# Performance work log

Hardware: AMD Instinct MI355X
Metric: run time of the kernel (lower is better)

Reference implementation:

```python
import jax, jax.numpy as jnp
import numpy as np


def _ln(x, g, b, eps=1e-5):
    m = x.mean(-1, keepdims=True)
    v = ((x - m) ** 2).mean(-1, keepdims=True)
    return (x - m) * jax.lax.rsqrt(v + eps) * g + b


def _forward(x, norm1_g, norm1_b, in_proj_w, conv_w, x_proj_w, dt_projs_w,
             dt_projs_b, A_logs, Ds, out_norm_g, out_norm_b, out_proj_w,
             norm2_g, norm2_b, fc1_w, fc1_b, fc2_w, fc2_b):
    B, C, H, W = x.shape
    z = jnp.transpose(x, (0, 2, 3, 1))  # (B,H,W,C)

    # ---- SS2D branch (forward_type='v3noz': no z gate) ----
    u = _ln(z, norm1_g, norm1_b)
    u = u @ in_proj_w.T                       # (B,H,W,Din)
    Din = u.shape[-1]
    uc = jnp.transpose(u, (0, 3, 1, 2))       # (B,Din,H,W)
    uc = jax.lax.conv_general_dilated(
        uc, conv_w, (1, 1), 'SAME', feature_group_count=Din,
        dimension_numbers=('NCHW', 'OIHW', 'NCHW'))
    uc = jax.nn.silu(uc)

    L = H * W
    K = x_proj_w.shape[0]                     # 4 scan directions
    R = dt_projs_w.shape[-1]                  # dt_rank
    N = (x_proj_w.shape[1] - R) // 2          # d_state

    # cross-scan: row-major, col-major, and their reversals
    xf = uc.reshape(B, Din, L)
    xt = jnp.transpose(uc, (0, 1, 3, 2)).reshape(B, Din, L)
    xs = jnp.stack([xf, xt, xf[..., ::-1], xt[..., ::-1]], axis=1)  # (B,K,Din,L)

    dbl = jnp.einsum('bkdl,kcd->bkcl', xs, x_proj_w)
    dts, Bs, Cs = jnp.split(dbl, [R, R + N], axis=2)  # (B,K,R,L),(B,K,N,L),(B,K,N,L)
    dt = jax.nn.softplus(jnp.einsum('bkrl,kdr->bkdl', dts, dt_projs_w)
                         + dt_projs_b[None, :, :, None])  # (B,K,Din,L)
    A = -jnp.exp(A_logs).reshape(K, Din, N)

    # selective scan: h_t = exp(dt*A)*h_{t-1} + dt*B_t*u_t; via associative scan
    a = jnp.exp(dt[:, :, :, None, :] * A[None, :, :, :, None])          # (B,K,Din,N,L)
    bb = dt[:, :, :, None, :] * Bs[:, :, None, :, :] * xs[:, :, :, None, :]

    def comb(e1, e2):
        a1, b1 = e1
        a2, b2 = e2
        return a2 * a1, a2 * b1 + b2

    _, h = jax.lax.associative_scan(comb, (a, bb), axis=-1)
    y = jnp.einsum('bkdnl,bknl->bkdl', h, Cs) + Ds.reshape(K, Din)[None, :, :, None] * xs

    # cross-merge: undo reversals / transpose, then sum
    yr = y[:, 0] + y[:, 2][..., ::-1]
    yt = jnp.transpose((y[:, 1] + y[:, 3][..., ::-1]).reshape(B, Din, W, H),
                       (0, 1, 3, 2)).reshape(B, Din, L)
    ym = jnp.transpose((yr + yt).reshape(B, Din, H, W), (0, 2, 3, 1))  # (B,H,W,Din)

    ym = _ln(ym, out_norm_g, out_norm_b)
    z = z + ym @ out_proj_w.T

    # ---- MLP branch ----
    m = _ln(z, norm2_g, norm2_b)
    m = jax.nn.gelu(m @ fc1_w.T + fc1_b, approximate=False) @ fc2_w.T + fc2_b
    z = z + m

    # outer wrapper residual
    return x + jnp.transpose(z, (0, 3, 1, 2))


def setup_inputs() -> dict:
    key = jax.random.key(0)
    ks = jax.random.split(key, 10)
    dims, Din, R, N, K, dmlp = 96, 192, 6, 1, 4, 384
    B, H, W = 4, 64, 64
    f32 = jnp.float32
    return {
        'x': jax.random.normal(ks[0], (B, dims, H, W), f32),
        'norm1_g': jnp.ones((dims,), f32),
        'norm1_b': jnp.zeros((dims,), f32),
        'in_proj_w': jax.random.normal(ks[1], (Din, dims), f32) * 0.02,
        'conv_w': jax.random.normal(ks[2], (Din, 1, 3, 3), f32) * 0.1,
        'x_proj_w': jax.random.normal(ks[3], (K, R + 2 * N, Din), f32) * 0.02,
        'dt_projs_w': jax.random.normal(ks[4], (K, Din, R), f32) * 0.1,
        'dt_projs_b': jax.random.uniform(ks[5], (K, Din), f32) * 0.1,
        'A_logs': jnp.zeros((K * Din, N), f32),  # v0 init: A=arange(1,N+1) -> log=0 for N=1
        'Ds': jnp.ones((K * Din,), f32),
        'out_norm_g': jnp.ones((Din,), f32),
        'out_norm_b': jnp.zeros((Din,), f32),
        'out_proj_w': jax.random.normal(ks[6], (dims, Din), f32) * 0.02,
        'norm2_g': jnp.ones((dims,), f32),
        'norm2_b': jnp.zeros((dims,), f32),
        'fc1_w': jax.random.normal(ks[7], (dmlp, dims), f32) * 0.02,
        'fc1_b': jnp.zeros((dmlp,), f32),
        'fc2_w': jax.random.normal(ks[8], (dims, dmlp), f32) * 0.02,
        'fc2_b': jnp.zeros((dims,), f32),
    }


def reference(x, norm1_g, norm1_b, in_proj_w, conv_w, x_proj_w, dt_projs_w,
              dt_projs_b, A_logs, Ds, out_norm_g, out_norm_b, out_proj_w,
              norm2_g, norm2_b, fc1_w, fc1_b, fc2_w, fc2_b):
    return _forward(x, norm1_g, norm1_b, in_proj_w, conv_w, x_proj_w,
                    dt_projs_w, dt_projs_b, A_logs, Ds, out_norm_g, out_norm_b,
                    out_proj_w, norm2_g, norm2_b, fc1_w, fc1_b, fc2_w, fc2_b)
```

## Files before the change

kernel.cpp:

```cpp
#include <hip/hip_runtime.h>
#include <math.h>

namespace {

constexpr int Bn = 4, Cn = 96, Hn = 64, Wn = 64, Ln = 4096, Din = 192;
constexpr int Kn = 4, Rn = 6, Dmlp = 384;
constexpr int NCH = 128, CLEN = 32;

typedef short short8 __attribute__((ext_vector_type(8)));
typedef float f32x4 __attribute__((ext_vector_type(4)));

__device__ __forceinline__ float softplusf_(float x) {
  return fmaxf(x, 0.f) + __logf(1.f + __expf(-fabsf(x)));
}
__device__ __forceinline__ float siluf_(float x) {
  return x / (1.f + __expf(-x));
}
__device__ __forceinline__ float geluf_(float x) {
  return 0.5f * x * (1.f + erff(x * 0.7071067811865476f));
}
__device__ __forceinline__ unsigned short f2bf(float f) {
  unsigned u = __float_as_uint(f);
  unsigned r = 0x7fffu + ((u >> 16) & 1u);
  return (unsigned short)((u + r) >> 16);
}
__device__ __forceinline__ float bf2f(unsigned short v) {
  return __uint_as_float(((unsigned)v) << 16);
}

__global__ __launch_bounds__(256) void k1_ln_inproj(
    const float* __restrict__ x, const float* __restrict__ gam,
    const float* __restrict__ bet, const float* __restrict__ win,
    const float* __restrict__ w1, const float* __restrict__ w2,
    const float* __restrict__ wout, const float* __restrict__ wxp,
    unsigned short* __restrict__ ucpb, unsigned short* __restrict__ w1b,
    unsigned short* __restrict__ w2b, unsigned short* __restrict__ woutb,
    unsigned short* __restrict__ wxpb) {
  const int tid = threadIdx.x;
  if (blockIdx.x >= 512) {
    int t = (blockIdx.x - 512) * 256 + tid;
    if (t < 36864) w1b[t] = f2bf(w1[t]);
    else if (t < 73728) w2b[t - 36864] = f2bf(w2[t - 36864]);
    else if (t < 92160) woutb[t - 73728] = f2bf(wout[t - 73728]);
    else wxpb[t - 92160] = f2bf(wxp[t - 92160]);
    return;
  }

  __shared__ float sx[32 * 97];
  __shared__ __align__(16) unsigned short smb[32 * 104];
  __shared__ __align__(16) unsigned short swin[192 * 96];
  const int p0 = blockIdx.x * 32;
  const int b = p0 >> 12, pl0 = p0 & (Ln - 1);

  for (int e = tid; e < 4608; e += 256) {
    float4 w4 = reinterpret_cast<const float4*>(win)[e];
    uint2 pk;
    pk.x = (unsigned)f2bf(w4.x) | ((unsigned)f2bf(w4.y) << 16);
    pk.y = (unsigned)f2bf(w4.z) | ((unsigned)f2bf(w4.w) << 16);
    *reinterpret_cast<uint2*>(&swin[e * 4]) = pk;
  }

  for (int f = tid; f < 32 * 96; f += 256) {
    int c = f >> 5, pp = f & 31;
    sx[pp * 97 + c] = x[((size_t)b * Cn + c) * Ln + pl0 + pp];
  }
  __syncthreads();
  {
    const int pp = tid >> 3, t8 = tid & 7;
    float s = 0.f;
    for (int c = t8 * 12; c < t8 * 12 + 12; ++c) s += sx[pp * 97 + c];
    s += __shfl_xor(s, 1, 8); s += __shfl_xor(s, 2, 8); s += __shfl_xor(s, 4, 8);
    float m = s * (1.f / 96.f);
    float v = 0.f;
    for (int c = t8 * 12; c < t8 * 12 + 12; ++c) {
      float t = sx[pp * 97 + c] - m; v += t * t;
    }
    v += __shfl_xor(v, 1, 8); v += __shfl_xor(v, 2, 8); v += __shfl_xor(v, 4, 8);
    float rs = rsqrtf(v * (1.f / 96.f) + 1e-5f);
    for (int c = t8 * 12; c < t8 * 12 + 12; ++c)
      sx[pp * 97 + c] = (sx[pp * 97 + c] - m) * rs * gam[c] + bet[c];
  }
  __syncthreads();
  for (int f = tid; f < 32 * 96; f += 256) {
    int pp = f / 96, c = f % 96;
    smb[pp * 104 + c] = f2bf(sx[pp * 97 + c]);
  }
  __syncthreads();

  const int wv = tid >> 6, lane = tid & 63;
  const int l15 = lane & 15, lhi = lane >> 4;
  const int mt = wv & 1, nbase = (wv >> 1) * 6;
  for (int t = 0; t < 6; ++t) {
    const int n0 = (nbase + t) * 16;
    f32x4 acc = {0.f, 0.f, 0.f, 0.f};
#pragma unroll
    for (int kk = 0; kk < 3; ++kk) {
      short8 av = *reinterpret_cast<const short8*>(
          &smb[(16 * mt + l15) * 104 + kk * 32 + lhi * 8]);
      short8 bv = *reinterpret_cast<const short8*>(
          &swin[(n0 + l15) * 96 + kk * 32 + lhi * 8]);
      acc = __builtin_amdgcn_mfma_f32_16x16x32_bf16(av, bv, acc, 0, 0, 0);
    }
    const int j = n0 + l15;
    uint2 pk;
    pk.x = (unsigned)f2bf(acc[0]) | ((unsigned)f2bf(acc[1]) << 16);
    pk.y = (unsigned)f2bf(acc[2]) | ((unsigned)f2bf(acc[3]) << 16);
    *reinterpret_cast<uint2*>(
        &ucpb[((size_t)b * Din + j) * Ln + pl0 + 16 * mt + lhi * 4]) = pk;
  }
}

__global__ __launch_bounds__(512) void k2a_conv(
    const unsigned short* __restrict__ ucpb, const float* __restrict__ cw,
    unsigned short* __restrict__ utb) {
  __shared__ float su[64 * 97];
  const int tid = threadIdx.x;
  const int bid = blockIdx.x;
  const int half = bid & 1, bh = bid >> 1;
  const int b = bh >> 6, h = bh & 63;
  const int w = tid & 63, wg = tid >> 6;
  const int d0 = half * 96;

  for (int dd = 0; dd < 12; ++dd) {
    int dl = wg * 12 + dd;
    int d = d0 + dl;
    const unsigned short* base = &ucpb[((size_t)b * Din + d) * Ln];
    float r0 = (h > 0) ? bf2f(base[(h - 1) * 64 + w]) : 0.f;
    float r1 = bf2f(base[h * 64 + w]);
    float r2 = (h < 63) ? bf2f(base[(h + 1) * 64 + w]) : 0.f;
    const float* wt = &cw[d * 9];
    float rl, rr, acc;
    rl = __shfl(r0, (w + 63) & 63); if (w == 0) rl = 0.f;
    rr = __shfl(r0, (w + 1) & 63);  if (w == 63) rr = 0.f;
    acc = rl * wt[0] + r0 * wt[1] + rr * wt[2];
    rl = __shfl(r1, (w + 63) & 63); if (w == 0) rl = 0.f;
    rr = __shfl(r1, (w + 1) & 63);  if (w == 63) rr = 0.f;
    acc += rl * wt[3] + r1 * wt[4] + rr * wt[5];
    rl = __shfl(r2, (w + 63) & 63); if (w == 0) rl = 0.f;
    rr = __shfl(r2, (w + 1) & 63);  if (w == 63) rr = 0.f;
    acc += rl * wt[6] + r2 * wt[7] + rr * wt[8];
    su[w * 97 + dl] = siluf_(acc);
  }
  __syncthreads();

  for (int f = tid; f < 768; f += 512) {
    int pp = f / 12, c8 = (f % 12) * 8;
    short8 v;
#pragma unroll
    for (int j = 0; j < 8; ++j) v[j] = (short)f2bf(su[pp * 97 + c8 + j]);
    *reinterpret_cast<short8*>(
        &utb[((size_t)b * Ln + h * 64 + pp) * Din + d0 + c8]) = v;
  }
}

__device__ __forceinline__ int scan_pixel(int k, int l) {
  if (k == 0) return l;
  if (k == 1) return ((l & 63) << 6) | (l >> 6);
  if (k == 2) return Ln - 1 - l;
  int m2 = Ln - 1 - l;
  return ((m2 & 63) << 6) | (m2 >> 6);
}

__device__ __forceinline__ void scan_stage(
    const unsigned short* __restrict__ ub,
    const unsigned short* __restrict__ wxpb, int k, int l0, int d,
    unsigned short* su, float* sdb) {
  for (int e = d; e < 768; e += 192) {
    int i = e / 24, c8 = (e % 24) * 8;
    int p = scan_pixel(k, l0 + i);
    *reinterpret_cast<short8*>(&su[i * 200 + c8]) =
        *reinterpret_cast<const short8*>(&ub[(size_t)p * 192 + c8]);
  }
  __syncthreads();
  const int wv3 = d >> 6, lane = d & 63;
  const int l15 = lane & 15, lhi = lane >> 4;
  if (wv3 < 2) {
    const int mt = wv3;
    const int n0 = (k >> 1) * 16;
    f32x4 acc = {0.f, 0.f, 0.f, 0.f};
#pragma unroll
    for (int kk = 0; kk < 6; ++kk) {
      short8 av = *reinterpret_cast<const short8*>(
          &su[(16 * mt + l15) * 200 + kk * 32 + lhi * 8]);
      short8 bv = *reinterpret_cast<const short8*>(
          &wxpb[(size_t)(n0 + l15) * 192 + kk * 32 + lhi * 8]);
      acc = __builtin_amdgcn_mfma_f32_16x16x32_bf16(av, bv, acc, 0, 0, 0);
    }
    if ((l15 >> 3) == (k & 1)) {
      const int c8 = l15 & 7;
#pragma unroll
      for (int r = 0; r < 4; ++r)
        sdb[(16 * mt + lhi * 4 + r) * 8 + c8] = acc[r];
    }
  }
  __syncthreads();
}

__global__ __launch_bounds__(192) void k4_scan1(
    const unsigned short* __restrict__ utb,
    const unsigned short* __restrict__ wxpb, const float* __restrict__ wdtg,
    const float* __restrict__ bdtg, const float* __restrict__ alog,
    float* __restrict__ apb, float* __restrict__ heb) {
  __shared__ __align__(16) unsigned short su[32 * 200];
  __shared__ __align__(16) float sdb[CLEN * 8];
  const int bid = blockIdx.x;
  const int ch = bid & (NCH - 1);
  const int bk = bid / NCH;
  const int b = bk >> 2, k = bk & 3;
  const int d = threadIdx.x;
  const int l0 = ch * CLEN;

  float wdt[6];
#pragma unroll
  for (int r = 0; r < 6; ++r) wdt[r] = wdtg[(k * Din + d) * 6 + r];
  const float bdt = bdtg[k * Din + d];
  const float Av = -__expf(alog[k * Din + d]);

  scan_stage(&utb[(size_t)b * Ln * Din], wxpb, k, l0, d, su, sdb);

  float h = 0.f, ap = 1.f;
  for (int i0 = 0; i0 < CLEN; i0 += 8) {
    float U[8];
#pragma unroll
    for (int j = 0; j < 8; ++j) U[j] = bf2f(su[(i0 + j) * 200 + d]);
#pragma unroll
    for (int j = 0; j < 8; ++j) {
      float4 qa = *reinterpret_cast<const float4*>(&sdb[(i0 + j) * 8]);
      float4 qb = *reinterpret_cast<const float4*>(&sdb[(i0 + j) * 8 + 4]);
      float xdt = bdt;
      xdt = fmaf(qa.x, wdt[0], xdt); xdt = fmaf(qa.y, wdt[1], xdt);
      xdt = fmaf(qa.z, wdt[2], xdt); xdt = fmaf(qa.w, wdt[3], xdt);
      xdt = fmaf(qb.x, wdt[4], xdt); xdt = fmaf(qb.y, wdt[5], xdt);
      float dt = softplusf_(xdt);
      float a = __expf(dt * Av);
      float bbv = dt * qb.z * U[j];
      h = fmaf(a, h, bbv);
      ap *= a;
    }
  }
  size_t o = ((size_t)bk * NCH + ch) * Din + d;
  apb[o] = ap;
  heb[o] = h;
}

__global__ __launch_bounds__(192) void k6_scan2(
    const unsigned short* __restrict__ utb,
    const unsigned short* __restrict__ wxpb, const float* __restrict__ wdtg,
    const float* __restrict__ bdtg, const float* __restrict__ alog,
    const float* __restrict__ dsg, const float* __restrict__ apb,
    const float* __restrict__ heb, unsigned short* __restrict__ yd) {
  __shared__ __align__(16) unsigned short su[32 * 200];
  __shared__ __align__(16) float sdb[CLEN * 8];
  __shared__ __align__(16) unsigned short ys[CLEN * 192];
  const int bid = blockIdx.x;
  const int ch = bid & (NCH - 1);
  const int bk = bid / NCH;
  const int b = bk >> 2, k = bk & 3;
  const int d = threadIdx.x;
  const int l0 = ch * CLEN;

  float wdt[6];
#pragma unroll
  for (int r = 0; r < 6; ++r) wdt[r] = wdtg[(k * Din + d) * 6 + r];
  const float bdt = bdtg[k * Din + d];
  const float Av = -__expf(alog[k * Din + d]);
  const float Dv = dsg[k * Din + d];
  unsigned short* yk = &yd[(size_t)bk * Ln * Din];

  float h = 0.f;
  {
    const float* ap_ = &apb[(size_t)bk * NCH * Din + d];
    const float* hp_ = &heb[(size_t)bk * NCH * Din + d];
    int j0 = 0;
    for (; j0 + 8 <= ch; j0 += 8) {
      float A[8], H[8];
#pragma unroll
      for (int jj = 0; jj < 8; ++jj) {
        A[jj] = ap_[(size_t)(j0 + jj) * Din];
        H[jj] = hp_[(size_t)(j0 + jj) * Din];
      }
#pragma unroll
      for (int jj = 0; jj < 8; ++jj) h = fmaf(A[jj], h, H[jj]);
    }
    for (; j0 < ch; ++j0)
      h = fmaf(ap_[(size_t)j0 * Din], h, hp_[(size_t)j0 * Din]);
  }

  scan_stage(&utb[(size_t)b * Ln * Din], wxpb, k, l0, d, su, sdb);

  for (int i0 = 0; i0 < CLEN; i0 += 8) {
    float U[8];
#pragma unroll
    for (int j = 0; j < 8; ++j) U[j] = bf2f(su[(i0 + j) * 200 + d]);
#pragma unroll
    for (int j = 0; j < 8; ++j) {
      float4 qa = *reinterpret_cast<const float4*>(&sdb[(i0 + j) * 8]);
      float4 qb = *reinterpret_cast<const float4*>(&sdb[(i0 + j) * 8 + 4]);
      float xdt = bdt;
      xdt = fmaf(qa.x, wdt[0], xdt); xdt = fmaf(qa.y, wdt[1], xdt);
      xdt = fmaf(qa.z, wdt[2], xdt); xdt = fmaf(qa.w, wdt[3], xdt);
      xdt = fmaf(qb.x, wdt[4], xdt); xdt = fmaf(qb.y, wdt[5], xdt);
      float dt = softplusf_(xdt);
      float a = __expf(dt * Av);
      float bbv = dt * qb.z * U[j];
      h = fmaf(a, h, bbv);
      ys[(i0 + j) * 192 + d] = f2bf(h * qb.w + Dv * U[j]);
    }
  }
  __syncthreads();
  for (int e = d; e < CLEN * 24; e += 192) {
    *reinterpret_cast<short8*>(&yk[(size_t)l0 * 192 + e * 8]) =
        *reinterpret_cast<const short8*>(&ys[e * 8]);
  }
}

__global__ __launch_bounds__(256) void k78_tail(
    const unsigned short* __restrict__ yd, const float* __restrict__ gam,
    const float* __restrict__ bet, const unsigned short* __restrict__ woutb,
    const float* __restrict__ g2, const float* __restrict__ b2,
    const unsigned short* __restrict__ w1b, const float* __restrict__ b1f,
    const unsigned short* __restrict__ w2b, const float* __restrict__ b2f,
    const float* __restrict__ x, float* __restrict__ out) {
  __shared__ __align__(16) char smem[50304];
  float* SY = (float*)smem;
  unsigned short* SB7 = (unsigned short*)(smem + 24704);
  unsigned short* SH = (unsigned short*)(smem + 37504);
  float* SZ = (float*)smem;
  unsigned short* SM = (unsigned short*)(smem + 12416);
  float* SMLP = (float*)(smem + 24704);

  const int tid = threadIdx.x;
  const int p0 = blockIdx.x * 32;
  const int b = p0 >> 12, pl0 = p0 & (Ln - 1);
  const int wv = tid >> 6, lane = tid & 63;
  const int l15 = lane & 15, lhi = lane >> 4;

  {
    const unsigned short* y0b = &yd[(size_t)(b * 4 + 0) * Ln * Din];
    const unsigned short* y1b = &yd[(size_t)(b * 4 + 1) * Ln * Din];
    const unsigned short* y2b = &yd[(size_t)(b * 4 + 2) * Ln * Din];
    const unsigned short* y3b = &yd[(size_t)(b * 4 + 3) * Ln * Din];
    for (int f = tid; f < 32 * 24; f += 256) {
      int pp = f / 24, c8 = (f % 24) * 8;
      int p = pl0 + pp;
      int l1 = ((p & 63) << 6) | (p >> 6);
      short8 v0 = *reinterpret_cast<const short8*>(&y0b[(size_t)p * 192 + c8]);
      short8 v2 = *reinterpret_cast<const short8*>(
          &y2b[(size_t)(Ln - 1 - p) * 192 + c8]);
      short8 v1 = *reinterpret_cast<const short8*>(&y1b[(size_t)l1 * 192 + c8]);
      short8 v3 = *reinterpret_cast<const short8*>(
          &y3b[(size_t)(Ln - 1 - l1) * 192 + c8]);
#pragma unroll
      for (int j = 0; j < 8; ++j)
        SY[pp * 193 + c8 + j] =
            bf2f((unsigned short)v0[j]) + bf2f((unsigned short)v2[j]) +
            bf2f((unsigned short)v1[j]) + bf2f((unsigned short)v3[j]);
    }
  }
  __syncthreads();

  {
    const int pp = tid >> 3, t8 = tid & 7;
    float s = 0.f;
    for (int d2 = t8 * 24; d2 < t8 * 24 + 24; ++d2) s += SY[pp * 193 + d2];
    s += __shfl_xor(s, 1, 8); s += __shfl_xor(s, 2, 8); s += __shfl_xor(s, 4, 8);
    float m = s * (1.f / 192.f);
    float v = 0.f;
    for (int d2 = t8 * 24; d2 < t8 * 24 + 24; ++d2) {
      float t = SY[pp * 193 + d2] - m; v += t * t;
    }
    v += __shfl_xor(v, 1, 8); v += __shfl_xor(v, 2, 8); v += __shfl_xor(v, 4, 8);
    float rs = rsqrtf(v * (1.f / 192.f) + 1e-5f);
    for (int d2 = t8 * 24; d2 < t8 * 24 + 24; ++d2)
      SB7[pp * 200 + d2] = f2bf((SY[pp * 193 + d2] - m) * rs * gam[d2] + bet[d2]);
  }
  __syncthreads();

  for (int q = 0; q < 3; ++q) {
    const int tt = wv + q * 4;
    const int mt = tt & 1, c0 = (tt >> 1) * 16;
    f32x4 acc = {0.f, 0.f, 0.f, 0.f};
#pragma unroll
    for (int kk = 0; kk < 6; ++kk) {
      short8 av = *reinterpret_cast<const short8*>(
          &SB7[(16 * mt + l15) * 200 + kk * 32 + lhi * 8]);
      short8 bv = *reinterpret_cast<const short8*>(
          &woutb[(size_t)(c0 + l15) * 192 + kk * 32 + lhi * 8]);
      acc = __builtin_amdgcn_mfma_f32_16x16x32_bf16(av, bv, acc, 0, 0, 0);
    }
    const int c = c0 + l15;
#pragma unroll
    for (int r = 0; r < 4; ++r) {
      int px = 16 * mt + lhi * 4 + r;
      SZ[px * 97 + c] = acc[r];
    }
  }
  __syncthreads();

  float xr[12];
#pragma unroll
  for (int it = 0; it < 12; ++it) {
    int f = tid + it * 256;
    int c = f >> 5, pp = f & 31;
    xr[it] = x[((size_t)b * Cn + c) * Ln + pl0 + pp];
    SZ[pp * 97 + c] += xr[it];
  }
  __syncthreads();

  {
    const int pp = tid >> 3, t8 = tid & 7;
    float s = 0.f;
    for (int c = t8 * 12; c < t8 * 12 + 12; ++c) s += SZ[pp * 97 + c];
    s += __shfl_xor(s, 1, 8); s += __shfl_xor(s, 2, 8); s += __shfl_xor(s, 4, 8);
    float m = s * (1.f / 96.f);
    float v = 0.f;
    for (int c = t8 * 12; c < t8 * 12 + 12; ++c) {
      float t = SZ[pp * 97 + c] - m; v += t * t;
    }
    v += __shfl_xor(v, 1, 8); v += __shfl_xor(v, 2, 8); v += __shfl_xor(v, 4, 8);
    float rs = rsqrtf(v * (1.f / 96.f) + 1e-5f);
    for (int c = t8 * 12; c < t8 * 12 + 12; ++c)
      SM[pp * 104 + c] = f2bf((SZ[pp * 97 + c] - m) * rs * g2[c] + b2[c]);
  }
  __syncthreads();

  f32x4 acc2[3];
#pragma unroll
  for (int q = 0; q < 3; ++q) acc2[q] = (f32x4){0.f, 0.f, 0.f, 0.f};

  for (int hlf = 0; hlf < 2; ++hlf) {
    {
      const int mt = wv & 1;
      const int ngrp = (wv >> 1) * 6;
      for (int t = 0; t < 6; ++t) {
        const int n0 = (ngrp + t) * 16;
        f32x4 acc = {0.f, 0.f, 0.f, 0.f};
#pragma unroll
        for (int kk = 0; kk < 3; ++kk) {
          short8 av = *reinterpret_cast<const short8*>(
              &SM[(16 * mt + l15) * 104 + kk * 32 + lhi * 8]);
          short8 bv = *reinterpret_cast<const short8*>(
              &w1b[(size_t)(hlf * 192 + n0 + l15) * 96 + kk * 32 + lhi * 8]);
          acc = __builtin_amdgcn_mfma_f32_16x16x32_bf16(av, bv, acc, 0, 0, 0);
        }
        const int jl = n0 + l15;
        const float bj = b1f[hlf * 192 + jl];
#pragma unroll
        for (int r = 0; r < 4; ++r) {
          int px = 16 * mt + lhi * 4 + r;
          SH[px * 200 + jl] = f2bf(geluf_(acc[r] + bj));
        }
      }
    }
    __syncthreads();
    for (int q = 0; q < 3; ++q) {
      const int tt = wv + q * 4;
      const int mt = tt & 1, c0 = (tt >> 1) * 16;
#pragma unroll
      for (int kk = 0; kk < 6; ++kk) {
        short8 av = *reinterpret_cast<const short8*>(
            &SH[(16 * mt + l15) * 200 + kk * 32 + lhi * 8]);
        short8 bv = *reinterpret_cast<const short8*>(
            &w2b[(size_t)(c0 + l15) * 384 + hlf * 192 + kk * 32 + lhi * 8]);
        acc2[q] = __builtin_amdgcn_mfma_f32_16x16x32_bf16(av, bv, acc2[q], 0, 0, 0);
      }
    }
    __syncthreads();
  }

  for (int q = 0; q < 3; ++q) {
    const int tt = wv + q * 4;
    const int mt = tt & 1, c0 = (tt >> 1) * 16;
    const int c = c0 + l15;
    const float bc = b2f[c];
#pragma unroll
    for (int r = 0; r < 4; ++r) {
      int px = 16 * mt + lhi * 4 + r;
      SMLP[px * 97 + c] = acc2[q][r] + bc;
    }
  }
  __syncthreads();

#pragma unroll
  for (int it = 0; it < 12; ++it) {
    int f = tid + it * 256;
    int c = f >> 5, pp = f & 31;
    out[((size_t)b * Cn + c) * Ln + pl0 + pp] =
        xr[it] + SZ[pp * 97 + c] + SMLP[pp * 97 + c];
  }
}

}

extern "C" void kernel_launch(void* const* d_in, const int* in_sizes, int n_in,
                              void* d_out, int out_size, void* d_ws,
                              size_t ws_size, hipStream_t stream) {
  const float* x        = (const float*)d_in[0];
  const float* norm1_g  = (const float*)d_in[1];
  const float* norm1_b  = (const float*)d_in[2];
  const float* in_proj  = (const float*)d_in[3];
  const float* conv_w   = (const float*)d_in[4];
  const float* x_proj   = (const float*)d_in[5];
  const float* dt_w     = (const float*)d_in[6];
  const float* dt_b     = (const float*)d_in[7];
  const float* A_logs   = (const float*)d_in[8];
  const float* Ds       = (const float*)d_in[9];
  const float* onorm_g  = (const float*)d_in[10];
  const float* onorm_b  = (const float*)d_in[11];
  const float* out_proj = (const float*)d_in[12];
  const float* norm2_g  = (const float*)d_in[13];
  const float* norm2_b  = (const float*)d_in[14];
  const float* fc1_w    = (const float*)d_in[15];
  const float* fc1_b    = (const float*)d_in[16];
  const float* fc2_w    = (const float*)d_in[17];
  const float* fc2_b    = (const float*)d_in[18];
  float* out = (float*)d_out;

  float* ws = (float*)d_ws;
  size_t o = 0;
  float* apb  = ws + o; o += (size_t)Bn * Kn * NCH * Din;
  float* heb  = ws + o; o += (size_t)Bn * Kn * NCH * Din;
  unsigned short* ucpb = (unsigned short*)(ws + o); o += (size_t)Bn * Din * Ln / 2;
  unsigned short* utb  = (unsigned short*)(ws + o); o += (size_t)Bn * Ln * Din / 2;
  unsigned short* yd   = (unsigned short*)(ws + o); o += (size_t)Bn * Kn * Ln * Din / 2;
  unsigned short* w1b = (unsigned short*)(ws + o); o += 36864 / 2;
  unsigned short* w2b = (unsigned short*)(ws + o); o += 36864 / 2;
  unsigned short* woutb = (unsigned short*)(ws + o); o += 18432 / 2;
  unsigned short* wxpb = (unsigned short*)(ws + o); o += 6144 / 2;

  k1_ln_inproj<<<896, 256, 0, stream>>>(x, norm1_g, norm1_b, in_proj, fc1_w,
                                        fc2_w, out_proj, x_proj, ucpb, w1b,
                                        w2b, woutb, wxpb);
  k2a_conv<<<Bn * Hn * 2, 512, 0, stream>>>(ucpb, conv_w, utb);
  k4_scan1<<<Bn * Kn * NCH, 192, 0, stream>>>(utb, wxpb, dt_w, dt_b, A_logs,
                                              apb, heb);
  k6_scan2<<<Bn * Kn * NCH, 192, 0, stream>>>(utb, wxpb, dt_w, dt_b, A_logs,
                                              Ds, apb, heb, yd);
  k78_tail<<<512, 256, 0, stream>>>(yd, onorm_g, onorm_b, woutb, norm2_g,
                                    norm2_b, w1b, fc1_b, w2b, fc2_b, x, out);
}
```

Measured before the change: 103.3 us.

## Replace two-pass chunked scan with single pass plus carry-correction in tail

The second scan pass, which recomputed the whole chunk scan with a carried-in state, is removed. The first pass now emits the zero-init local output y together with a per-position factor P·C. A tiny carry kernel computes each chunk's incoming state serially, and the tail kernel adds y + (P·C)·carry when merging directions. This drops the duplicated projection and scan recompute. In exchange it writes and reads an extra bf16 tensor the size of yd, and it stores the prefix product in bf16, which adds rounding error.

```diff
diff --git a/kernel.cpp b/kernel.cpp
--- a/kernel.cpp
+++ b/kernel.cpp
@@ -196,13 +196,16 @@
   __syncthreads();
 }
 
-__global__ __launch_bounds__(192) void k4_scan1(
+__global__ __launch_bounds__(192) void k4_scanY(
     const unsigned short* __restrict__ utb,
     const unsigned short* __restrict__ wxpb, const float* __restrict__ wdtg,
     const float* __restrict__ bdtg, const float* __restrict__ alog,
-    float* __restrict__ apb, float* __restrict__ heb) {
+    const float* __restrict__ dsg, float* __restrict__ apb,
+    float* __restrict__ heb, unsigned short* __restrict__ yd,
+    unsigned short* __restrict__ pcg) {
   __shared__ __align__(16) unsigned short su[32 * 200];
   __shared__ __align__(16) float sdb[CLEN * 8];
+  __shared__ __align__(16) unsigned short ys[CLEN * 192];
   const int bid = blockIdx.x;
   const int ch = bid & (NCH - 1);
   const int bk = bid / NCH;
@@ -215,10 +218,13 @@
   for (int r = 0; r < 6; ++r) wdt[r] = wdtg[(k * Din + d) * 6 + r];
   const float bdt = bdtg[k * Din + d];
   const float Av = -__expf(alog[k * Din + d]);
+  const float Dv = dsg[k * Din + d];
+  unsigned short* yk = &yd[(size_t)bk * Ln * Din];
+  unsigned short* pk = &pcg[(size_t)bk * Ln * Din];
 
   scan_stage(&utb[(size_t)b * Ln * Din], wxpb, k, l0, d, su, sdb);
 
-  float h = 0.f, ap = 1.f;
+  float h = 0.f, P = 1.f;
   for (int i0 = 0; i0 < CLEN; i0 += 8) {
     float U[8];
 #pragma unroll
@@ -235,78 +241,14 @@
       float a = __expf(dt * Av);
       float bbv = dt * qb.z * U[j];
       h = fmaf(a, h, bbv);
-      ap *= a;
+      P *= a;
+      ys[(i0 + j) * 192 + d] = f2bf(h * qb.w + Dv * U[j]);
+      pk[(size_t)(l0 + i0 + j) * 192 + d] = f2bf(P * qb.w);
     }
   }
   size_t o = ((size_t)bk * NCH + ch) * Din + d;
-  apb[o] = ap;
+  apb[o] = P;
   heb[o] = h;
-}
-
-__global__ __launch_bounds__(192) void k6_scan2(
-    const unsigned short* __restrict__ utb,
-    const unsigned short* __restrict__ wxpb, const float* __restrict__ wdtg,
-    const float* __restrict__ bdtg, const float* __restrict__ alog,
-    const float* __restrict__ dsg, const float* __restrict__ apb,
-    const float* __restrict__ heb, unsigned short* __restrict__ yd) {
-  __shared__ __align__(16) unsigned short su[32 * 200];
-  __shared__ __align__(16) float sdb[CLEN * 8];
-  __shared__ __align__(16) unsigned short ys[CLEN * 192];
-  const int bid = blockIdx.x;
-  const int ch = bid & (NCH - 1);
-  const int bk = bid / NCH;
-  const int b = bk >> 2, k = bk & 3;
-  const int d = threadIdx.x;
-  const int l0 = ch * CLEN;
-
-  float wdt[6];
-#pragma unroll
-  for (int r = 0; r < 6; ++r) wdt[r] = wdtg[(k * Din + d) * 6 + r];
-  const float bdt = bdtg[k * Din + d];
-  const float Av = -__expf(alog[k * Din + d]);
-  const float Dv = dsg[k * Din + d];
-  unsigned short* yk = &yd[(size_t)bk * Ln * Din];
-
-  float h = 0.f;
-  {
-    const float* ap_ = &apb[(size_t)bk * NCH * Din + d];
-    const float* hp_ = &heb[(size_t)bk * NCH * Din + d];
-    int j0 = 0;
-    for (; j0 + 8 <= ch; j0 += 8) {
-      float A[8], H[8];
-#pragma unroll
-      for (int jj = 0; jj < 8; ++jj) {
-        A[jj] = ap_[(size_t)(j0 + jj) * Din];
-        H[jj] = hp_[(size_t)(j0 + jj) * Din];
-      }
-#pragma unroll
-      for (int jj = 0; jj < 8; ++jj) h = fmaf(A[jj], h, H[jj]);
-    }
-    for (; j0 < ch; ++j0)
-      h = fmaf(ap_[(size_t)j0 * Din], h, hp_[(size_t)j0 * Din]);
-  }
-
-  scan_stage(&utb[(size_t)b * Ln * Din], wxpb, k, l0, d, su, sdb);
-
-  for (int i0 = 0; i0 < CLEN; i0 += 8) {
-    float U[8];
-#pragma unroll
-    for (int j = 0; j < 8; ++j) U[j] = bf2f(su[(i0 + j) * 200 + d]);
-#pragma unroll
-    for (int j = 0; j < 8; ++j) {
-      float4 qa = *reinterpret_cast<const float4*>(&sdb[(i0 + j) * 8]);
-      float4 qb = *reinterpret_cast<const float4*>(&sdb[(i0 + j) * 8 + 4]);
-      float xdt = bdt;
-      xdt = fmaf(qa.x, wdt[0], xdt); xdt = fmaf(qa.y, wdt[1], xdt);
-      xdt = fmaf(qa.z, wdt[2], xdt); xdt = fmaf(qa.w, wdt[3], xdt);
-      xdt = fmaf(qb.x, wdt[4], xdt); xdt = fmaf(qb.y, wdt[5], xdt);
-      float dt = softplusf_(xdt);
-      float a = __expf(dt * Av);
-      float bbv = dt * qb.z * U[j];
-      h = fmaf(a, h, bbv);
-      ys[(i0 + j) * 192 + d] = f2bf(h * qb.w + Dv * U[j]);
-    }
-  }
   __syncthreads();
   for (int e = d; e < CLEN * 24; e += 192) {
     *reinterpret_cast<short8*>(&yk[(size_t)l0 * 192 + e * 8]) =
@@ -314,13 +256,29 @@
   }
 }
 
+__global__ __launch_bounds__(256) void k5_carry(
+    const float* __restrict__ apb, const float* __restrict__ heb,
+    float* __restrict__ cin) {
+  int t = blockIdx.x * 256 + threadIdx.x;
+  if (t >= Bn * Kn * Din) return;
+  int bk = t / Din, d = t % Din;
+  float c = 0.f;
+  for (int ch = 0; ch < NCH; ++ch) {
+    size_t o = ((size_t)bk * NCH + ch) * Din + d;
+    cin[o] = c;
+    c = fmaf(apb[o], c, heb[o]);
+  }
+}
+
 __global__ __launch_bounds__(256) void k78_tail(
-    const unsigned short* __restrict__ yd, const float* __restrict__ gam,
-    const float* __restrict__ bet, const unsigned short* __restrict__ woutb,
-    const float* __restrict__ g2, const float* __restrict__ b2,
-    const unsigned short* __restrict__ w1b, const float* __restrict__ b1f,
-    const unsigned short* __restrict__ w2b, const float* __restrict__ b2f,
-    const float* __restrict__ x, float* __restrict__ out) {
+    const unsigned short* __restrict__ yd,
+    const unsigned short* __restrict__ pcg, const float* __restrict__ cin,
+    const float* __restrict__ gam, const float* __restrict__ bet,
+    const unsigned short* __restrict__ woutb, const float* __restrict__ g2,
+    const float* __restrict__ b2, const unsigned short* __restrict__ w1b,
+    const float* __restrict__ b1f, const unsigned short* __restrict__ w2b,
+    const float* __restrict__ b2f, const float* __restrict__ x,
+    float* __restrict__ out) {
   __shared__ __align__(16) char smem[50304];
   float* SY = (float*)smem;
   unsigned short* SB7 = (unsigned short*)(smem + 24704);
@@ -335,27 +293,32 @@
   const int wv = tid >> 6, lane = tid & 63;
   const int l15 = lane & 15, lhi = lane >> 4;
 
-  {
-    const unsigned short* y0b = &yd[(size_t)(b * 4 + 0) * Ln * Din];
-    const unsigned short* y1b = &yd[(size_t)(b * 4 + 1) * Ln * Din];
-    const unsigned short* y2b = &yd[(size_t)(b * 4 + 2) * Ln * Din];
-    const unsigned short* y3b = &yd[(size_t)(b * 4 + 3) * Ln * Din];
-    for (int f = tid; f < 32 * 24; f += 256) {
-      int pp = f / 24, c8 = (f % 24) * 8;
-      int p = pl0 + pp;
-      int l1 = ((p & 63) << 6) | (p >> 6);
-      short8 v0 = *reinterpret_cast<const short8*>(&y0b[(size_t)p * 192 + c8]);
-      short8 v2 = *reinterpret_cast<const short8*>(
-          &y2b[(size_t)(Ln - 1 - p) * 192 + c8]);
-      short8 v1 = *reinterpret_cast<const short8*>(&y1b[(size_t)l1 * 192 + c8]);
-      short8 v3 = *reinterpret_cast<const short8*>(
-          &y3b[(size_t)(Ln - 1 - l1) * 192 + c8]);
+  for (int f = tid; f < 32 * 24; f += 256) {
+    int pp = f / 24, c8 = (f % 24) * 8;
+    int p = pl0 + pp;
+    int l1 = ((p & 63) << 6) | (p >> 6);
+    float s[8];
+#pragma unroll
+    for (int j = 0; j < 8; ++j) s[j] = 0.f;
+#pragma unroll
+    for (int k = 0; k < 4; ++k) {
+      int l = (k == 0) ? p : (k == 1) ? l1 : (k == 2) ? (Ln - 1 - p)
+                                                      : (Ln - 1 - l1);
+      size_t base = ((size_t)(b * 4 + k) * Ln + l) * 192 + c8;
+      short8 py = *reinterpret_cast<const short8*>(&yd[base]);
+      short8 pc = *reinterpret_cast<const short8*>(&pcg[base]);
+      const float* cp =
+          &cin[((size_t)(b * 4 + k) * NCH + (l >> 5)) * 192 + c8];
+      float4 ca = *reinterpret_cast<const float4*>(cp);
+      float4 cb = *reinterpret_cast<const float4*>(cp + 4);
+      float cv[8] = {ca.x, ca.y, ca.z, ca.w, cb.x, cb.y, cb.z, cb.w};
 #pragma unroll
       for (int j = 0; j < 8; ++j)
-        SY[pp * 193 + c8 + j] =
-            bf2f((unsigned short)v0[j]) + bf2f((unsigned short)v2[j]) +
-            bf2f((unsigned short)v1[j]) + bf2f((unsigned short)v3[j]);
-    }
+        s[j] += bf2f((unsigned short)py[j]) +
+                bf2f((unsigned short)pc[j]) * cv[j];
+    }
+#pragma unroll
+    for (int j = 0; j < 8; ++j) SY[pp * 193 + c8 + j] = s[j];
   }
   __syncthreads();
 
@@ -520,9 +483,11 @@
   size_t o = 0;
   float* apb  = ws + o; o += (size_t)Bn * Kn * NCH * Din;
   float* heb  = ws + o; o += (size_t)Bn * Kn * NCH * Din;
+  float* cin  = ws + o; o += (size_t)Bn * Kn * NCH * Din;
   unsigned short* ucpb = (unsigned short*)(ws + o); o += (size_t)Bn * Din * Ln / 2;
   unsigned short* utb  = (unsigned short*)(ws + o); o += (size_t)Bn * Ln * Din / 2;
   unsigned short* yd   = (unsigned short*)(ws + o); o += (size_t)Bn * Kn * Ln * Din / 2;
+  unsigned short* pcg  = (unsigned short*)(ws + o); o += (size_t)Bn * Kn * Ln * Din / 2;
   unsigned short* w1b = (unsigned short*)(ws + o); o += 36864 / 2;
   unsigned short* w2b = (unsigned short*)(ws + o); o += 36864 / 2;
   unsigned short* woutb = (unsigned short*)(ws + o); o += 18432 / 2;
@@ -532,10 +497,10 @@
                                         fc2_w, out_proj, x_proj, ucpb, w1b,
                                         w2b, woutb, wxpb);
   k2a_conv<<<Bn * Hn * 2, 512, 0, stream>>>(ucpb, conv_w, utb);
-  k4_scan1<<<Bn * Kn * NCH, 192, 0, stream>>>(utb, wxpb, dt_w, dt_b, A_logs,
-                                              apb, heb);
-  k6_scan2<<<Bn * Kn * NCH, 192, 0, stream>>>(utb, wxpb, dt_w, dt_b, A_logs,
-                                              Ds, apb, heb, yd);
-  k78_tail<<<512, 256, 0, stream>>>(yd, onorm_g, onorm_b, woutb, norm2_g,
-                                    norm2_b, w1b, fc1_b, w2b, fc2_b, x, out);
-}
+  k4_scanY<<<Bn * Kn * NCH, 192, 0, stream>>>(utb, wxpb, dt_w, dt_b, A_logs,
+                                              Ds, apb, heb, yd, pcg);
+  k5_carry<<<12, 256, 0, stream>>>(apb, heb, cin);
+  k78_tail<<<512, 256, 0, stream>>>(yd, pcg, cin, onorm_g, onorm_b, woutb,
+                                    norm2_g, norm2_b, w1b, fc1_b, w2b, fc2_b,
+                                    x, out);
+}
```

Result: no change. 101.8 us (-1.5%).
